# Optimization experiments

Hardware: AMD Instinct MI355X
Metric: run time of the kernel (lower is better)

The kernel has to match this reference:

```python
import jax, jax.numpy as jnp
import numpy as np

N = 50000
E = 800000
IN_C = 64
OUT_C = 128
T = 4


def setup_inputs() -> dict:
    key = jax.random.key(0)
    ks = jax.random.split(key, 12)
    s = 0.05
    return {
        "x": jax.random.normal(ks[0], (N, IN_C), dtype=jnp.float32),
        "u": jax.random.normal(ks[1], (N, OUT_C), dtype=jnp.float32),
        "edge_index": jax.random.randint(ks[2], (2, E), 0, N, dtype=jnp.int32),
        # w1: Linear(in_channels, out_channels)
        "w1_W": jax.random.normal(ks[3], (OUT_C, IN_C), dtype=jnp.float32) * s,
        "w1_b": jnp.zeros((OUT_C,), dtype=jnp.float32),
        # sigmod MLP: three Linear(out, out) layers
        "m1_W": jax.random.normal(ks[4], (OUT_C, OUT_C), dtype=jnp.float32) * s,
        "m1_b": jnp.zeros((OUT_C,), dtype=jnp.float32),
        "m2_W": jax.random.normal(ks[5], (OUT_C, OUT_C), dtype=jnp.float32) * s,
        "m2_b": jnp.zeros((OUT_C,), dtype=jnp.float32),
        "m3_W": jax.random.normal(ks[6], (OUT_C, OUT_C), dtype=jnp.float32) * s,
        "m3_b": jnp.zeros((OUT_C,), dtype=jnp.float32),
        # w2: Linear(out, out) for graph readout
        "w2_W": jax.random.normal(ks[7], (OUT_C, OUT_C), dtype=jnp.float32) * s,
        "w2_b": jnp.zeros((OUT_C,), dtype=jnp.float32),
    }


def reference(x, u, edge_index, w1_W, w1_b, m1_W, m1_b, m2_W, m2_b, m3_W, m3_b, w2_W, w2_b):
    n_nodes = x.shape[0]
    src = edge_index[0]  # gather source (u_j)
    dst = edge_index[1]  # scatter-add target
    xw = x @ w1_W.T + w1_b  # [N, out]; identical every iteration
    for _ in range(T):
        agg = jax.ops.segment_sum(u[src], dst, num_segments=n_nodes)  # [N, out]
        h = jax.nn.relu(agg @ m1_W.T + m1_b)
        h = jax.nn.relu(h @ m2_W.T + m2_b)
        h = jnp.tanh(h @ m3_W.T + m3_b)
        u = jax.nn.relu(xw + h)
    g = jnp.sum(u, axis=0, keepdims=True)  # e @ u with e = ones [1, N]
    return g @ w2_W.T + w2_b  # [1, out]
```

## Files before the change

### kernel.cpp

```cpp
#include <hip/hip_runtime.h>
#include <hip/hip_bf16.h>

#define NN 50000
#define NE 800000
#define CI 64
#define CO 128
#define NB 196
#define CHUNK 2048
#define NCH 391

typedef __attribute__((ext_vector_type(8))) short bf16x8;
typedef __attribute__((ext_vector_type(4))) float f32x4;

__device__ __forceinline__ unsigned short f2bf(float f) {
  unsigned int u = __float_as_uint(f);
  u += 0x7fffu + ((u >> 16) & 1u);
  return (unsigned short)(u >> 16);
}
__device__ __forceinline__ float bf2f_lo(unsigned int p) { return __uint_as_float(p << 16); }
__device__ __forceinline__ float bf2f_hi(unsigned int p) { return __uint_as_float(p & 0xffff0000u); }
__device__ __forceinline__ unsigned int pk2(float lo, float hi) {
  return ((unsigned int)f2bf(hi) << 16) | (unsigned int)f2bf(lo);
}

__global__ __launch_bounds__(256) void k_bhist(const int* __restrict__ dst,
                                               int* __restrict__ bcnt) {
  __shared__ int lc[NB];
  int tid = threadIdx.x;
  for (int t = tid; t < NB; t += 256) lc[t] = 0;
  __syncthreads();
  int base = blockIdx.x * CHUNK;
#pragma unroll
  for (int i = 0; i < 8; ++i) {
    int idx = base + i * 256 + tid;
    if (idx < NE) atomicAdd(&lc[dst[idx] >> 8], 1);
  }
  __syncthreads();
  for (int t = tid; t < NB; t += 256) if (lc[t]) atomicAdd(&bcnt[t], lc[t]);
}

__global__ __launch_bounds__(256) void k_bscan(const int* __restrict__ bcnt,
                                               int* __restrict__ bkt_off,
                                               int* __restrict__ bkt_cur) {
  __shared__ int s[256];
  int t = threadIdx.x;
  int v = (t < NB) ? bcnt[t] : 0;
  s[t] = v;
  __syncthreads();
  for (int off = 1; off < 256; off <<= 1) {
    int x = (t >= off) ? s[t - off] : 0;
    __syncthreads();
    s[t] += x;
    __syncthreads();
  }
  if (t < NB) { int e = s[t] - v; bkt_off[t] = e; bkt_cur[t] = e; }
  if (t == 0) bkt_off[NB] = NE;
}

__global__ __launch_bounds__(256) void k_bin(const int* __restrict__ src,
                                             const int* __restrict__ dst,
                                             int* __restrict__ bkt_cur,
                                             uint2* __restrict__ pairs) {
  __shared__ int lcnt[NB];
  __shared__ int lbase[NB];
  int tid = threadIdx.x;
  for (int t = tid; t < NB; t += 256) lcnt[t] = 0;
  __syncthreads();
  int base = blockIdx.x * CHUNK;
  int ds[8], sr[8], rk[8];
#pragma unroll
  for (int i = 0; i < 8; ++i) {
    int idx = base + i * 256 + tid;
    if (idx < NE) {
      ds[i] = dst[idx]; sr[i] = src[idx];
      rk[i] = atomicAdd(&lcnt[ds[i] >> 8], 1);
    } else ds[i] = -1;
  }
  __syncthreads();
  for (int t = tid; t < NB; t += 256)
    lbase[t] = lcnt[t] ? atomicAdd(&bkt_cur[t], lcnt[t]) : 0;
  __syncthreads();
#pragma unroll
  for (int i = 0; i < 8; ++i) {
    if (ds[i] >= 0) {
      uint2 pr; pr.x = (unsigned)sr[i]; pr.y = (unsigned)ds[i];
      pairs[lbase[ds[i] >> 8] + rk[i]] = pr;
    }
  }
}

__global__ __launch_bounds__(256) void k_fillB(const uint2* __restrict__ pairs,
                                               const int* __restrict__ bkt_off,
                                               int* __restrict__ row_off,
                                               int* __restrict__ ssrc) {
  __shared__ int lc[256];
  __shared__ int ls[256];
  int t = threadIdx.x, b = blockIdx.x;
  lc[t] = 0;
  __syncthreads();
  int beg = bkt_off[b], end = bkt_off[b + 1];
  for (int i = beg + t; i < end; i += 256)
    atomicAdd(&lc[pairs[i].y & 255], 1);
  __syncthreads();
  int v = lc[t];
  ls[t] = v;
  __syncthreads();
  for (int off = 1; off < 256; off <<= 1) {
    int x = (t >= off) ? ls[t - off] : 0;
    __syncthreads();
    ls[t] += x;
    __syncthreads();
  }
  int excl = ls[t] - v;
  int node = (b << 8) + t;
  if (node < NN) row_off[node] = beg + excl;
  if (b == 0 && t == 0) row_off[NN] = NE;
  lc[t] = beg + excl;
  __syncthreads();
  for (int i = beg + t; i < end; i += 256) {
    uint2 e = pairs[i];
    int pos = atomicAdd(&lc[e.y & 255], 1);
    ssrc[pos] = (int)e.x;
  }
}

__global__ __launch_bounds__(256) void k_cvt(const float* __restrict__ w1,
    const float* __restrict__ m1, const float* __restrict__ m2,
    const float* __restrict__ m3, unsigned short* __restrict__ wb,
    const float* __restrict__ u0, unsigned short* __restrict__ ub) {
  int i = blockIdx.x * 256 + threadIdx.x;
  if (i < 14336) {
    int i4 = i * 4;
    float4 v;
    if (i4 < 8192)       v = *(const float4*)(w1 + i4);
    else if (i4 < 24576) v = *(const float4*)(m1 + i4 - 8192);
    else if (i4 < 40960) v = *(const float4*)(m2 + i4 - 24576);
    else                 v = *(const float4*)(m3 + i4 - 40960);
    ushort2 lo = { f2bf(v.x), f2bf(v.y) };
    ushort2 hi = { f2bf(v.z), f2bf(v.w) };
    *(ushort2*)(wb + i4) = lo;
    *(ushort2*)(wb + i4 + 2) = hi;
  }
  if (i < NN * CO / 4) {
    float4 v = *(const float4*)(u0 + i * 4);
    ushort2 lo = { f2bf(v.x), f2bf(v.y) };
    ushort2 hi = { f2bf(v.z), f2bf(v.w) };
    *(ushort2*)(ub + i * 4) = lo;
    *(ushort2*)(ub + i * 4 + 2) = hi;
  }
}

__global__ __launch_bounds__(256) void k_gather(const int* __restrict__ row_off,
    const int* __restrict__ ssrc, const unsigned short* __restrict__ ubf,
    unsigned short* __restrict__ agg) {
  int wave = threadIdx.x >> 6, lane = threadIdx.x & 63;
  int g = lane >> 4, c = lane & 15;
  int node = blockIdx.x * 16 + wave * 4 + g;
  int gl = g << 4;
  int beg = row_off[node], end = row_off[node + 1];
  float a[8];
#pragma unroll
  for (int i = 0; i < 8; ++i) a[i] = 0.f;

#define ADD8(r) { a[0] += bf2f_lo(r.x); a[1] += bf2f_hi(r.x); \
                  a[2] += bf2f_lo(r.y); a[3] += bf2f_hi(r.y); \
                  a[4] += bf2f_lo(r.z); a[5] += bf2f_hi(r.z); \
                  a[6] += bf2f_lo(r.w); a[7] += bf2f_hi(r.w); }

  for (int base = beg; base < end; base += 16) {
    int e = base + c;
    int sid = (e < end) ? ssrc[e] : 0;
    int cnt = min(16, end - base);
    int j = 0;
    for (; j + 8 <= cnt; j += 8) {
      int s0 = __shfl(sid, gl + j + 0);
      int s1 = __shfl(sid, gl + j + 1);
      int s2 = __shfl(sid, gl + j + 2);
      int s3 = __shfl(sid, gl + j + 3);
      int s4 = __shfl(sid, gl + j + 4);
      int s5 = __shfl(sid, gl + j + 5);
      int s6 = __shfl(sid, gl + j + 6);
      int s7 = __shfl(sid, gl + j + 7);
      uint4 r0 = *(const uint4*)(ubf + (size_t)s0 * CO + c * 8);
      uint4 r1 = *(const uint4*)(ubf + (size_t)s1 * CO + c * 8);
      uint4 r2 = *(const uint4*)(ubf + (size_t)s2 * CO + c * 8);
      uint4 r3 = *(const uint4*)(ubf + (size_t)s3 * CO + c * 8);
      uint4 r4 = *(const uint4*)(ubf + (size_t)s4 * CO + c * 8);
      uint4 r5 = *(const uint4*)(ubf + (size_t)s5 * CO + c * 8);
      uint4 r6 = *(const uint4*)(ubf + (size_t)s6 * CO + c * 8);
      uint4 r7 = *(const uint4*)(ubf + (size_t)s7 * CO + c * 8);
      ADD8(r0); ADD8(r1); ADD8(r2); ADD8(r3);
      ADD8(r4); ADD8(r5); ADD8(r6); ADD8(r7);
    }
    for (; j + 4 <= cnt; j += 4) {
      int s0 = __shfl(sid, gl + j + 0);
      int s1 = __shfl(sid, gl + j + 1);
      int s2 = __shfl(sid, gl + j + 2);
      int s3 = __shfl(sid, gl + j + 3);
      uint4 r0 = *(const uint4*)(ubf + (size_t)s0 * CO + c * 8);
      uint4 r1 = *(const uint4*)(ubf + (size_t)s1 * CO + c * 8);
      uint4 r2 = *(const uint4*)(ubf + (size_t)s2 * CO + c * 8);
      uint4 r3 = *(const uint4*)(ubf + (size_t)s3 * CO + c * 8);
      ADD8(r0); ADD8(r1); ADD8(r2); ADD8(r3);
    }
    for (; j < cnt; ++j) {
      int s = __shfl(sid, gl + j);
      uint4 r = *(const uint4*)(ubf + (size_t)s * CO + c * 8);
      ADD8(r);
    }
  }
#undef ADD8
  uint4 o;
  o.x = pk2(a[0], a[1]); o.y = pk2(a[2], a[3]);
  o.z = pk2(a[4], a[5]); o.w = pk2(a[6], a[7]);
  *(uint4*)(agg + (size_t)node * CO + c * 8) = o;
}

__global__ __launch_bounds__(256) void k_xw(const float* __restrict__ X,
    const unsigned short* __restrict__ W, const float* __restrict__ bias,
    unsigned short* __restrict__ xwb) {
  int wave = threadIdx.x >> 6, lane = threadIdx.x & 63;
  int m = lane & 15, q = lane >> 4;
  int row0 = blockIdx.x * 64 + wave * 16;
  int arow = row0 + m; if (arow >= NN) arow = NN - 1;
  const float* Xr = X + (size_t)arow * CI;
  f32x4 acc[8];
#pragma unroll
  for (int tt = 0; tt < 8; ++tt) acc[tt] = (f32x4){0.f, 0.f, 0.f, 0.f};
#pragma unroll
  for (int ks = 0; ks < CI; ks += 32) {
    float4 f0 = *(const float4*)(Xr + ks + q * 8);
    float4 f1 = *(const float4*)(Xr + ks + q * 8 + 4);
    union { unsigned int u[4]; bf16x8 v; } cv;
    cv.u[0] = pk2(f0.x, f0.y); cv.u[1] = pk2(f0.z, f0.w);
    cv.u[2] = pk2(f1.x, f1.y); cv.u[3] = pk2(f1.z, f1.w);
    bf16x8 a = cv.v;
#pragma unroll
    for (int tt = 0; tt < 8; ++tt) {
      bf16x8 b = *(const bf16x8*)(W + (size_t)(tt * 16 + m) * CI + ks + q * 8);
      acc[tt] = __builtin_amdgcn_mfma_f32_16x16x32_bf16(a, b, acc[tt], 0, 0, 0);
    }
  }
#pragma unroll
  for (int tt = 0; tt < 8; ++tt) {
    int o = tt * 16 + m;
    float bv = bias[o];
#pragma unroll
    for (int r = 0; r < 4; ++r) {
      int node = row0 + q * 4 + r;
      if (node < NN) xwb[(size_t)node * CO + o] = f2bf(acc[tt][r] + bv);
    }
  }
}

__global__ __launch_bounds__(512, 4) void k_mlp(const unsigned short* __restrict__ agg,
    const unsigned short* __restrict__ W1, const unsigned short* __restrict__ W2,
    const unsigned short* __restrict__ W3,
    const float* __restrict__ b1, const float* __restrict__ b2, const float* __restrict__ b3,
    const unsigned short* __restrict__ xwb, unsigned short* __restrict__ uout) {
  constexpr int SP = 136;
  __shared__ unsigned short lds[16384 + 8 * 16 * SP];
  unsigned short* wt = lds;
  int tid = threadIdx.x;
  int wave = tid >> 6, lane = tid & 63;
  int m = lane & 15, q = lane >> 4;
  int row0 = blockIdx.x * 128 + wave * 16;
  unsigned short* L = lds + 16384 + wave * 16 * SP;
  int ar = row0 + m; if (ar >= NN) ar = NN - 1;
  const unsigned short* Ap = agg + (size_t)ar * CO;

  uint4 wreg[4];
  const int trb = (tid >> 4) & 7;
  const int tc  = tid & 15;
  const int ldst0 = (tid >> 4) * 128 + ((tc ^ trb) << 3);
  auto stage_load = [&](const unsigned short* W) {
#pragma unroll
    for (int j = 0; j < 4; ++j)
      wreg[j] = *(const uint4*)(W + ((j * 512 + tid) << 3));
  };
  auto stage_write = [&]() {
#pragma unroll
    for (int j = 0; j < 4; ++j)
      *(uint4*)(wt + ldst0 + j * 4096) = wreg[j];
  };
  auto bfrag = [&](int t, int ks) -> bf16x8 {
    int ch = (ks >> 3) + q;
    return *(const bf16x8*)(wt + (t * 16 + m) * 128 + ((ch ^ (m & 7)) << 3));
  };

  stage_load(W1);
  bf16x8 ar4[4];
#pragma unroll
  for (int k4 = 0; k4 < 4; ++k4) ar4[k4] = *(const bf16x8*)(Ap + k4 * 32 + q * 8);
  stage_write();

  f32x4 acc[8];
#pragma unroll
  for (int t = 0; t < 8; ++t) acc[t] = (f32x4){0.f, 0.f, 0.f, 0.f};
  __syncthreads();

#pragma unroll
  for (int k4 = 0; k4 < 4; ++k4) {
#pragma unroll
    for (int t = 0; t < 8; ++t) {
      bf16x8 b = bfrag(t, k4 * 32);
      acc[t] = __builtin_amdgcn_mfma_f32_16x16x32_bf16(ar4[k4], b, acc[t], 0, 0, 0);
    }
  }
  stage_load(W2);
#pragma unroll
  for (int t = 0; t < 8; ++t) {
    float bv = b1[t * 16 + m];
#pragma unroll
    for (int r = 0; r < 4; ++r)
      L[(q * 4 + r) * SP + t * 16 + m] = f2bf(fmaxf(acc[t][r] + bv, 0.f));
  }
  __syncthreads();
  stage_write();
#pragma unroll
  for (int t = 0; t < 8; ++t) acc[t] = (f32x4){0.f, 0.f, 0.f, 0.f};
  __syncthreads();

#pragma unroll
  for (int ks = 0; ks < CO; ks += 32) {
    bf16x8 a = *(const bf16x8*)(L + m * SP + ks + q * 8);
#pragma unroll
    for (int t = 0; t < 8; ++t) {
      bf16x8 b = bfrag(t, ks);
      acc[t] = __builtin_amdgcn_mfma_f32_16x16x32_bf16(a, b, acc[t], 0, 0, 0);
    }
  }
  stage_load(W3);
#pragma unroll
  for (int t = 0; t < 8; ++t) {
    float bv = b2[t * 16 + m];
#pragma unroll
    for (int r = 0; r < 4; ++r)
      L[(q * 4 + r) * SP + t * 16 + m] = f2bf(fmaxf(acc[t][r] + bv, 0.f));
  }
  __syncthreads();
  stage_write();
#pragma unroll
  for (int t = 0; t < 8; ++t) acc[t] = (f32x4){0.f, 0.f, 0.f, 0.f};
  __syncthreads();

#pragma unroll
  for (int ks = 0; ks < CO; ks += 32) {
    bf16x8 a = *(const bf16x8*)(L + m * SP + ks + q * 8);
#pragma unroll
    for (int t = 0; t < 8; ++t) {
      bf16x8 b = bfrag(t, ks);
      acc[t] = __builtin_amdgcn_mfma_f32_16x16x32_bf16(a, b, acc[t], 0, 0, 0);
    }
  }
#pragma unroll
  for (int t = 0; t < 8; ++t) {
    float bv = b3[t * 16 + m];
#pragma unroll
    for (int r = 0; r < 4; ++r) {
      float v = acc[t][r] + bv;
      float e = __expf(2.f * v);
      v = 1.f - 2.f / (e + 1.f);
      L[(q * 4 + r) * SP + t * 16 + m] = f2bf(v);
    }
  }
  int ln = lane >> 2, lc = lane & 3;
  int gnode = row0 + ln;
  if (gnode < NN) {
    const unsigned short* xr = xwb + (size_t)gnode * CO;
    unsigned short* ur = uout + (size_t)gnode * CO;
#pragma unroll
    for (int rnd = 0; rnd < 4; ++rnd) {
      int ch = (rnd * 4 + lc) * 8;
      uint4 h = *(const uint4*)(L + ln * SP + ch);
      uint4 xv = *(const uint4*)(xr + ch);
      uint4 o;
      o.x = pk2(fmaxf(bf2f_lo(h.x) + bf2f_lo(xv.x), 0.f), fmaxf(bf2f_hi(h.x) + bf2f_hi(xv.x), 0.f));
      o.y = pk2(fmaxf(bf2f_lo(h.y) + bf2f_lo(xv.y), 0.f), fmaxf(bf2f_hi(h.y) + bf2f_hi(xv.y), 0.f));
      o.z = pk2(fmaxf(bf2f_lo(h.z) + bf2f_lo(xv.z), 0.f), fmaxf(bf2f_hi(h.z) + bf2f_hi(xv.z), 0.f));
      o.w = pk2(fmaxf(bf2f_lo(h.w) + bf2f_lo(xv.w), 0.f), fmaxf(bf2f_hi(h.w) + bf2f_hi(xv.w), 0.f));
      *(uint4*)(ur + ch) = o;
    }
  }
}

__global__ __launch_bounds__(256) void k_reduce(const unsigned short* __restrict__ u,
                                                float* __restrict__ g) {
  int ch2 = threadIdx.x & 63;
  int sub = threadIdx.x >> 6;
  float a0 = 0.f, a1 = 0.f;
  for (int n = blockIdx.x * 4 + sub; n < NN; n += gridDim.x * 4) {
    unsigned int p = *(const unsigned int*)(u + (size_t)n * CO + ch2 * 2);
    a0 += bf2f_lo(p); a1 += bf2f_hi(p);
  }
  __shared__ float s0[256], s1[256];
  s0[threadIdx.x] = a0; s1[threadIdx.x] = a1;
  __syncthreads();
  if (sub == 0) {
    a0 = s0[ch2] + s0[64 + ch2] + s0[128 + ch2] + s0[192 + ch2];
    a1 = s1[ch2] + s1[64 + ch2] + s1[128 + ch2] + s1[192 + ch2];
    atomicAdd(&g[ch2 * 2], a0);
    atomicAdd(&g[ch2 * 2 + 1], a1);
  }
}

__global__ void k_final(const float* __restrict__ g, const float* __restrict__ w2,
                        const float* __restrict__ b2, float* __restrict__ outp) {
  __shared__ float sg[128];
  if (threadIdx.x < 128) sg[threadIdx.x] = g[threadIdx.x];
  __syncthreads();
  int j = threadIdx.x;
  if (j < 128) {
    float acc = b2[j];
    for (int c = 0; c < 128; ++c) acc += sg[c] * w2[j * 128 + c];
    outp[j] = acc;
  }
}

extern "C" void kernel_launch(void* const* d_in, const int* in_sizes, int n_in,
                              void* d_out, int out_size, void* d_ws, size_t ws_size,
                              hipStream_t stream) {
  (void)in_sizes; (void)n_in; (void)out_size; (void)ws_size;
  const float* x   = (const float*)d_in[0];
  const float* u0  = (const float*)d_in[1];
  const int*   ei  = (const int*)d_in[2];
  const float* w1W = (const float*)d_in[3];
  const float* w1b = (const float*)d_in[4];
  const float* m1W = (const float*)d_in[5];
  const float* m1b = (const float*)d_in[6];
  const float* m2W = (const float*)d_in[7];
  const float* m2b = (const float*)d_in[8];
  const float* m3W = (const float*)d_in[9];
  const float* m3b = (const float*)d_in[10];
  const float* w2W = (const float*)d_in[11];
  const float* w2b = (const float*)d_in[12];
  const int* esrc = ei;
  const int* edst = ei + NE;

  char* p = (char*)d_ws;
  auto carve = [&](size_t bytes) { char* r = p; p += (bytes + 255) & ~(size_t)255; return r; };
  unsigned short* xwb     = (unsigned short*)carve((size_t)NN * CO * 2);
  unsigned short* ubf     = (unsigned short*)carve((size_t)NN * CO * 2);
  unsigned short* agg     = (unsigned short*)carve((size_t)NN * CO * 2);
  unsigned short* wbf     = (unsigned short*)carve((size_t)57344 * 2);
  int*            row_off = (int*)carve((size_t)(NN + 1) * 4);
  int*            ssrc    = (int*)carve((size_t)NE * 4);
  uint2*          pairs   = (uint2*)carve((size_t)NE * 8);
  int*            bkt_cnt = (int*)carve((size_t)NB * 4);
  int*            bkt_off = (int*)carve((size_t)(NB + 1) * 4);
  int*            bkt_cur = (int*)carve((size_t)NB * 4);
  float*          g       = (float*)carve(128 * 4);

  hipMemsetAsync(bkt_cnt, 0, (size_t)NB * 4, stream);
  hipMemsetAsync(g, 0, 128 * 4, stream);

  k_bhist<<<NCH, 256, 0, stream>>>(edst, bkt_cnt);
  k_bscan<<<1, 256, 0, stream>>>(bkt_cnt, bkt_off, bkt_cur);
  k_bin<<<NCH, 256, 0, stream>>>(esrc, edst, bkt_cur, pairs);
  k_fillB<<<NB, 256, 0, stream>>>(pairs, bkt_off, row_off, ssrc);

  k_cvt<<<(NN * CO / 4 + 255) / 256, 256, 0, stream>>>(w1W, m1W, m2W, m3W, wbf, u0, ubf);

  k_xw<<<(NN + 63) / 64, 256, 0, stream>>>(x, wbf, w1b, xwb);

  const unsigned short* Wm1 = wbf + 8192;
  const unsigned short* Wm2 = wbf + 8192 + 16384;
  const unsigned short* Wm3 = wbf + 8192 + 2 * 16384;
  const int GM = (NN + 127) / 128;
  for (int it = 0; it < 4; ++it) {
    k_gather<<<NN / 16, 256, 0, stream>>>(row_off, ssrc, ubf, agg);
    k_mlp<<<GM, 512, 0, stream>>>(agg, Wm1, Wm2, Wm3, m1b, m2b, m3b, xwb, ubf);
  }

  k_reduce<<<256, 256, 0, stream>>>(ubf, g);
  k_final<<<1, 128, 0, stream>>>(g, w2W, w2b, (float*)d_out);
}
```

Measured before the change: 404.4 us.

## Fuse scan and final GEMV via last-block pattern, pack edge pairs, trim gather unroll

Merges the bucket scan into the histogram kernel and the final w2 GEMV into the reduction kernel using an atomic done-counter so the last block finishes the work, removing two launches and a memset. Edge pairs are packed into a single 32-bit word (src<<8 | dst low byte), halving binning traffic. The 8-wide unrolled gather loop is dropped in favor of the 4-wide loop, reducing registers but also memory-level parallelism in the dominant gather kernel.

```diff
diff --git a/kernel.cpp b/kernel.cpp
--- a/kernel.cpp
+++ b/kernel.cpp
@@ -24,8 +24,12 @@
 }
 
 __global__ __launch_bounds__(256) void k_bhist(const int* __restrict__ dst,
-                                               int* __restrict__ bcnt) {
+                                               int* __restrict__ bcnt,
+                                               int* __restrict__ bkt_off,
+                                               int* __restrict__ bkt_cur,
+                                               int* __restrict__ done) {
   __shared__ int lc[NB];
+  __shared__ int lastblk;
   int tid = threadIdx.x;
   for (int t = tid; t < NB; t += 256) lc[t] = 0;
   __syncthreads();
@@ -37,14 +41,15 @@
   }
   __syncthreads();
   for (int t = tid; t < NB; t += 256) if (lc[t]) atomicAdd(&bcnt[t], lc[t]);
-}
-
-__global__ __launch_bounds__(256) void k_bscan(const int* __restrict__ bcnt,
-                                               int* __restrict__ bkt_off,
-                                               int* __restrict__ bkt_cur) {
+  __threadfence();
+  __syncthreads();
+  if (tid == 0) lastblk = (atomicAdd(done, 1) == NCH - 1);
+  __syncthreads();
+  if (!lastblk) return;
+  __threadfence();
   __shared__ int s[256];
-  int t = threadIdx.x;
-  int v = (t < NB) ? bcnt[t] : 0;
+  int t = tid;
+  int v = (t < NB) ? atomicAdd(&bcnt[t], 0) : 0;
   s[t] = v;
   __syncthreads();
   for (int off = 1; off < 256; off <<= 1) {
@@ -60,7 +65,7 @@
 __global__ __launch_bounds__(256) void k_bin(const int* __restrict__ src,
                                              const int* __restrict__ dst,
                                              int* __restrict__ bkt_cur,
-                                             uint2* __restrict__ pairs) {
+                                             unsigned* __restrict__ pairs) {
   __shared__ int lcnt[NB];
   __shared__ int lbase[NB];
   int tid = threadIdx.x;
@@ -82,14 +87,13 @@
   __syncthreads();
 #pragma unroll
   for (int i = 0; i < 8; ++i) {
-    if (ds[i] >= 0) {
-      uint2 pr; pr.x = (unsigned)sr[i]; pr.y = (unsigned)ds[i];
-      pairs[lbase[ds[i] >> 8] + rk[i]] = pr;
-    }
-  }
-}
-
-__global__ __launch_bounds__(256) void k_fillB(const uint2* __restrict__ pairs,
+    if (ds[i] >= 0)
+      pairs[lbase[ds[i] >> 8] + rk[i]] =
+          ((unsigned)sr[i] << 8) | (unsigned)(ds[i] & 255);
+  }
+}
+
+__global__ __launch_bounds__(256) void k_fillB(const unsigned* __restrict__ pairs,
                                                const int* __restrict__ bkt_off,
                                                int* __restrict__ row_off,
                                                int* __restrict__ ssrc) {
@@ -100,7 +104,7 @@
   __syncthreads();
   int beg = bkt_off[b], end = bkt_off[b + 1];
   for (int i = beg + t; i < end; i += 256)
-    atomicAdd(&lc[pairs[i].y & 255], 1);
+    atomicAdd(&lc[pairs[i] & 255], 1);
   __syncthreads();
   int v = lc[t];
   ls[t] = v;
@@ -118,9 +122,9 @@
   lc[t] = beg + excl;
   __syncthreads();
   for (int i = beg + t; i < end; i += 256) {
-    uint2 e = pairs[i];
-    int pos = atomicAdd(&lc[e.y & 255], 1);
-    ssrc[pos] = (int)e.x;
+    unsigned e = pairs[i];
+    int pos = atomicAdd(&lc[e & 255], 1);
+    ssrc[pos] = (int)(e >> 8);
   }
 }
 
@@ -172,26 +176,6 @@
     int sid = (e < end) ? ssrc[e] : 0;
     int cnt = min(16, end - base);
     int j = 0;
-    for (; j + 8 <= cnt; j += 8) {
-      int s0 = __shfl(sid, gl + j + 0);
-      int s1 = __shfl(sid, gl + j + 1);
-      int s2 = __shfl(sid, gl + j + 2);
-      int s3 = __shfl(sid, gl + j + 3);
-      int s4 = __shfl(sid, gl + j + 4);
-      int s5 = __shfl(sid, gl + j + 5);
-      int s6 = __shfl(sid, gl + j + 6);
-      int s7 = __shfl(sid, gl + j + 7);
-      uint4 r0 = *(const uint4*)(ubf + (size_t)s0 * CO + c * 8);
-      uint4 r1 = *(const uint4*)(ubf + (size_t)s1 * CO + c * 8);
-      uint4 r2 = *(const uint4*)(ubf + (size_t)s2 * CO + c * 8);
-      uint4 r3 = *(const uint4*)(ubf + (size_t)s3 * CO + c * 8);
-      uint4 r4 = *(const uint4*)(ubf + (size_t)s4 * CO + c * 8);
-      uint4 r5 = *(const uint4*)(ubf + (size_t)s5 * CO + c * 8);
-      uint4 r6 = *(const uint4*)(ubf + (size_t)s6 * CO + c * 8);
-      uint4 r7 = *(const uint4*)(ubf + (size_t)s7 * CO + c * 8);
-      ADD8(r0); ADD8(r1); ADD8(r2); ADD8(r3);
-      ADD8(r4); ADD8(r5); ADD8(r6); ADD8(r7);
-    }
     for (; j + 4 <= cnt; j += 4) {
       int s0 = __shfl(sid, gl + j + 0);
       int s1 = __shfl(sid, gl + j + 1);
@@ -385,7 +369,11 @@
 }
 
 __global__ __launch_bounds__(256) void k_reduce(const unsigned short* __restrict__ u,
-                                                float* __restrict__ g) {
+                                                float* __restrict__ g,
+                                                const float* __restrict__ w2,
+                                                const float* __restrict__ b2,
+                                                float* __restrict__ outp,
+                                                int* __restrict__ done) {
   int ch2 = threadIdx.x & 63;
   int sub = threadIdx.x >> 6;
   float a0 = 0.f, a1 = 0.f;
@@ -402,12 +390,15 @@
     atomicAdd(&g[ch2 * 2], a0);
     atomicAdd(&g[ch2 * 2 + 1], a1);
   }
-}
-
-__global__ void k_final(const float* __restrict__ g, const float* __restrict__ w2,
-                        const float* __restrict__ b2, float* __restrict__ outp) {
+  __threadfence();
+  __syncthreads();
+  __shared__ int lastblk;
+  if (threadIdx.x == 0) lastblk = (atomicAdd(done, 1) == (int)gridDim.x - 1);
+  __syncthreads();
+  if (!lastblk) return;
+  __threadfence();
   __shared__ float sg[128];
-  if (threadIdx.x < 128) sg[threadIdx.x] = g[threadIdx.x];
+  if (threadIdx.x < 128) sg[threadIdx.x] = atomicAdd(&g[threadIdx.x], 0.f);
   __syncthreads();
   int j = threadIdx.x;
   if (j < 128) {
@@ -445,17 +436,17 @@
   unsigned short* wbf     = (unsigned short*)carve((size_t)57344 * 2);
   int*            row_off = (int*)carve((size_t)(NN + 1) * 4);
   int*            ssrc    = (int*)carve((size_t)NE * 4);
-  uint2*          pairs   = (uint2*)carve((size_t)NE * 8);
-  int*            bkt_cnt = (int*)carve((size_t)NB * 4);
+  unsigned*       pairs   = (unsigned*)carve((size_t)NE * 4);
   int*            bkt_off = (int*)carve((size_t)(NB + 1) * 4);
   int*            bkt_cur = (int*)carve((size_t)NB * 4);
+  char*           zbase   = carve((size_t)NB * 4);
+  int*            bkt_cnt = (int*)zbase;
   float*          g       = (float*)carve(128 * 4);
-
-  hipMemsetAsync(bkt_cnt, 0, (size_t)NB * 4, stream);
-  hipMemsetAsync(g, 0, 128 * 4, stream);
-
-  k_bhist<<<NCH, 256, 0, stream>>>(edst, bkt_cnt);
-  k_bscan<<<1, 256, 0, stream>>>(bkt_cnt, bkt_off, bkt_cur);
+  int*            done    = (int*)carve(8);
+
+  hipMemsetAsync(zbase, 0, 1792, stream);
+
+  k_bhist<<<NCH, 256, 0, stream>>>(edst, bkt_cnt, bkt_off, bkt_cur, done);
   k_bin<<<NCH, 256, 0, stream>>>(esrc, edst, bkt_cur, pairs);
   k_fillB<<<NB, 256, 0, stream>>>(pairs, bkt_off, row_off, ssrc);
 
@@ -472,6 +463,5 @@
     k_mlp<<<GM, 512, 0, stream>>>(agg, Wm1, Wm2, Wm3, m1b, m2b, m3b, xwb, ubf);
   }
 
-  k_reduce<<<256, 256, 0, stream>>>(ubf, g);
-  k_final<<<1, 128, 0, stream>>>(g, w2W, w2b, (float*)d_out);
-}
+  k_reduce<<<256, 256, 0, stream>>>(ubf, g, w2W, w2b, (float*)d_out, done + 1);
+}
```

Measured after the change: 417.1 us. +3.2%, slower.
